# Kernel tuning notes

Hardware: AMD Instinct MI355X
Metric: run time of the kernel (lower is better)

Reference implementation:

```python
import jax, jax.numpy as jnp
import numpy as np

B, N, F = 2048, 65536, 128
NUM_K = 3
NUM_LABELS = 10
EXPONENT = 2.0


def setup_inputs() -> dict:
    key = jax.random.key(0)
    k1, k2, k3 = jax.random.split(key, 3)
    # positive inputs: tf.pow with a float exponent NaNs on negative bases
    x_input = jax.random.uniform(k1, (B, F), dtype=jnp.float32)
    train_inputs = jax.random.uniform(k2, (N, F), dtype=jnp.float32)
    train_labels = jax.random.randint(k3, (N,), 0, NUM_LABELS, dtype=jnp.int32)
    features = jnp.ones((F,), dtype=jnp.float32)  # abe_features, ones init
    return {
        "x_input": x_input,
        "train_inputs": train_inputs,
        "train_labels": train_labels,
        "features": features,
    }


def reference(x_input, train_inputs, train_labels, features):
    # weighted_inputs = features * train_inputs
    w = features[None, :] * train_inputs  # [N, F]

    # Minkowsky distance (faithful to the TF graph):
    # (sum(x^p) + sum(w^p))^(1/p) - 2 * x @ w^T
    left = jnp.sum(x_input ** EXPONENT, axis=1)[:, None]   # [B, 1]
    right = jnp.sum(w ** EXPONENT, axis=1)[None, :]        # [1, N]
    distance = (left + right) ** (1.0 / EXPONENT) - 2.0 * (x_input @ w.T)  # [B, N]

    # top-k nearest neighbors via top_k of negated distances
    values, indices = jax.lax.top_k(-distance, NUM_K)      # [B, K]

    # gather neighbor labels and average (tf.reduce_mean on int = floor div)
    labels = train_labels[indices]                          # [B, K] int32
    outputs = jnp.sum(labels, axis=1) // NUM_K              # [B] int32
    one_hot = jax.nn.one_hot(outputs, NUM_LABELS, dtype=jnp.float32)  # [B, NUM_LABELS]

    return (one_hot, values, indices, labels)
```

## Files before the change

### kernel.cpp

```cpp
#include <hip/hip_runtime.h>
#include <hip/hip_bf16.h>
#include <cstdint>
#include <cstddef>

typedef short bf16x8 __attribute__((ext_vector_type(8)));
typedef float f32x4 __attribute__((ext_vector_type(4)));

namespace {
constexpr int kB = 2048;
constexpr int kN = 65536;
constexpr int kF = 128;
constexpr int kLabels = 10;
constexpr int kIMax = 0x7fffffff;

constexpr int BM = 256;
constexpr int BN = 256;
constexpr int SLICE = 2048;
constexpr int NTILES = SLICE / BN;
constexpr int NCH = 12;
constexpr int NCHT = NTILES * NCH;
constexpr int NSUB = kN / 32;
constexpr float kMargin = 0.05f;
}

#define TOP3_INSERT(dd, ii, D0, I0, D1, I1, D2, I2)                              \
  do {                                                                           \
    float _d = (dd); int _i = (ii);                                              \
    if (_d < (D0) || (_d == (D0) && _i < (I0))) {                                \
      (D2) = (D1); (I2) = (I1); (D1) = (D0); (I1) = (I0); (D0) = _d; (I0) = _i;  \
    } else if (_d < (D1) || (_d == (D1) && _i < (I1))) {                         \
      (D2) = (D1); (I2) = (I1); (D1) = _d; (I1) = _i;                            \
    } else if (_d < (D2) || (_d == (D2) && _i < (I2))) {                         \
      (D2) = _d; (I2) = _i;                                                      \
    }                                                                            \
  } while (0)

__device__ inline unsigned short f2bf(float a) {
  __hip_bfloat16 h = __float2bfloat16(a);
  return __builtin_bit_cast(unsigned short, h);
}
__device__ inline float bf2f(unsigned short u) {
  return __bfloat162float(__builtin_bit_cast(__hip_bfloat16, u));
}

__device__ inline void gload_lds16(const void* g, void* l) {
  __builtin_amdgcn_global_load_lds(
      (const __attribute__((address_space(1))) void*)g,
      (__attribute__((address_space(3))) void*)l, 16, 0, 0);
}

__global__ __launch_bounds__(256) void pack_sumsq_kernel(
    const float* __restrict__ x, const float* __restrict__ train,
    const float* __restrict__ features, unsigned short* __restrict__ Ap,
    unsigned short* __restrict__ Bp, float* __restrict__ left,
    float* __restrict__ right) {
  const int wid = (int)((blockIdx.x * 256 + threadIdx.x) >> 6);
  const int lane = threadIdx.x & 63;
  if (wid >= kB + kN) return;
  const float2 fv = reinterpret_cast<const float2*>(features)[lane];
  const float* src;
  unsigned short* dst;
  float pm0, pm1, sm0, sm1;
  if (wid < kB) {
    src = x + (size_t)wid * kF;
    dst = Ap + (size_t)wid * 256;
    pm0 = fv.x; pm1 = fv.y;
    sm0 = 1.0f; sm1 = 1.0f;
  } else {
    src = train + (size_t)(wid - kB) * kF;
    dst = Bp + (size_t)(wid - kB) * 256;
    pm0 = 1.0f; pm1 = 1.0f;
    sm0 = fv.x; sm1 = fv.y;
  }
  const float2 v = reinterpret_cast<const float2*>(src)[lane];
  const float pa = v.x * pm0, pb = v.y * pm1;
  const float sa = v.x * sm0, sb = v.y * sm1;
  const unsigned short ha = f2bf(pa), hb = f2bf(pb);
  const unsigned short la = f2bf(pa - bf2f(ha)), lb = f2bf(pb - bf2f(hb));
  reinterpret_cast<unsigned int*>(dst)[lane] = (unsigned int)ha | ((unsigned int)hb << 16);
  reinterpret_cast<unsigned int*>(dst + 128)[lane] = (unsigned int)la | ((unsigned int)lb << 16);
  float s = sa * sa + sb * sb;
  #pragma unroll
  for (int m = 1; m <= 32; m <<= 1) s += __shfl_xor(s, m);
  if (lane == 0) {
    if (wid < kB) left[wid] = s;
    else right[wid - kB] = s;
  }
}

__global__ __launch_bounds__(512, 2) void knn_main_kernel(
    const unsigned short* __restrict__ Ap, const unsigned short* __restrict__ Bp,
    const float* __restrict__ left, const float* __restrict__ right,
    float* __restrict__ minbuf) {
  __shared__ alignas(16) unsigned short lsA[4][BM * 32];
  __shared__ alignas(16) unsigned short lsB[4][BN * 32];
  __shared__ alignas(16) float lsR[SLICE];

  const int slice = blockIdx.x;
  const int mb = blockIdx.y;
  const int row0 = mb * BM;
  const int col0 = slice * SLICE;
  const int t = threadIdx.x;
  const int lane = t & 63;
  const int wm = (t >> 6) >> 1;
  const int wn = (t >> 6) & 1;

  reinterpret_cast<float4*>(lsR)[t] =
      reinterpret_cast<const float4*>(right + col0)[t];

  float lrow[4][4];
  #pragma unroll
  for (int mf = 0; mf < 4; ++mf)
    #pragma unroll
    for (int rg = 0; rg < 4; ++rg)
      lrow[mf][rg] = left[row0 + wm * 64 + mf * 16 + (lane >> 4) * 4 + rg];

  const int rA = t >> 2;
  const int p = t & 3;
  size_t gbaseA[2], gbaseB[2];
  int ldsoff[2];
  #pragma unroll
  for (int i = 0; i < 2; ++i) {
    const int r = i * 128 + rA;
    const int ps = p ^ ((r >> 1) & 3);
    gbaseA[i] = (size_t)(row0 + r) * 512 + (size_t)ps * 16;
    gbaseB[i] = (size_t)(col0 + r) * 512 + (size_t)ps * 16;
    ldsoff[i] = i * 8192 + t * 16;
  }

  int offA[4], offB[8];
  #pragma unroll
  for (int mf = 0; mf < 4; ++mf) {
    const int rl = wm * 64 + mf * 16 + (lane & 15);
    offA[mf] = rl * 64 + (((lane >> 4) ^ ((rl >> 1) & 3)) * 16);
  }
  #pragma unroll
  for (int nf = 0; nf < 8; ++nf) {
    const int cl = wn * 128 + nf * 16 + (lane & 15);
    offB[nf] = cl * 64 + (((lane >> 4) ^ ((cl >> 1) & 3)) * 16);
  }

  const char* ApB = (const char*)Ap;
  const char* BpB = (const char*)Bp;

  auto stage = [&](int buf, int c, int nt) {
    const int skA = (c < 4) ? c * 32 : ((c < 8) ? 128 + (c - 4) * 32 : (c - 8) * 32);
    const int skB = (c < 4) ? c * 32 : ((c < 8) ? (c - 4) * 32 : 128 + (c - 8) * 32);
    char* lA = (char*)&lsA[buf][0];
    char* lB = (char*)&lsB[buf][0];
    #pragma unroll
    for (int i = 0; i < 2; ++i) {
      gload_lds16(ApB + gbaseA[i] + (size_t)skA * 2, lA + ldsoff[i]);
      gload_lds16(BpB + gbaseB[i] + (size_t)nt * 131072 + (size_t)skB * 2, lB + ldsoff[i]);
    }
  };

  asm volatile("s_waitcnt vmcnt(0) lgkmcnt(0)" ::: "memory");
  __syncthreads();

  int pn = 0, pc = 0;
  #pragma unroll
  for (int i = 0; i < 3; ++i) {
    stage(i, pc, pn);
    if (++pc == NCH) { pc = 0; ++pn; }
  }

  const bool bwriter = (lane & 3) == 0;

  int g = 0;
  for (int nt = 0; nt < NTILES; ++nt) {
    f32x4 acc[4][8];
    #pragma unroll
    for (int mf = 0; mf < 4; ++mf)
      #pragma unroll
      for (int nf = 0; nf < 8; ++nf)
        acc[mf][nf] = (f32x4){0.f, 0.f, 0.f, 0.f};

    for (int c = 0; c < NCH; ++c, ++g) {
      if (g + 3 < NCHT) {
        stage((g + 3) & 3, pc, pn);
        if (++pc == NCH) { pc = 0; ++pn; }
      }
      {
        const int rem = NCHT - 1 - g;
        if (rem >= 3)      asm volatile("s_waitcnt vmcnt(12)" ::: "memory");
        else if (rem == 2) asm volatile("s_waitcnt vmcnt(8)" ::: "memory");
        else if (rem == 1) asm volatile("s_waitcnt vmcnt(4)" ::: "memory");
        else               asm volatile("s_waitcnt vmcnt(0)" ::: "memory");
      }
      __builtin_amdgcn_s_barrier();
      asm volatile("" ::: "memory");

      const char* lA = (const char*)&lsA[g & 3][0];
      const char* lB = (const char*)&lsB[g & 3][0];
      bf16x8 a[4], b[8];
      #pragma unroll
      for (int mf = 0; mf < 4; ++mf)
        a[mf] = *reinterpret_cast<const bf16x8*>(lA + offA[mf]);
      #pragma unroll
      for (int nf = 0; nf < 8; ++nf)
        b[nf] = *reinterpret_cast<const bf16x8*>(lB + offB[nf]);
      __builtin_amdgcn_s_setprio(1);
      #pragma unroll
      for (int mf = 0; mf < 4; ++mf)
        #pragma unroll
        for (int nf = 0; nf < 8; ++nf)
          acc[mf][nf] = __builtin_amdgcn_mfma_f32_16x16x32_bf16(
              a[mf], b[nf], acc[mf][nf], 0, 0, 0);
      __builtin_amdgcn_s_setprio(0);
      asm volatile("" ::: "memory");
      __builtin_amdgcn_s_barrier();
      asm volatile("" ::: "memory");
    }

    float rj[8];
    #pragma unroll
    for (int nf = 0; nf < 8; ++nf)
      rj[nf] = lsR[nt * 256 + wn * 128 + nf * 16 + (lane & 15)];
    const int binbase = slice * 64 + nt * 8 + wn * 4 + ((lane >> 2) & 3);
    #pragma unroll
    for (int mf = 0; mf < 4; ++mf) {
      #pragma unroll
      for (int rg = 0; rg < 4; ++rg) {
        const float l = lrow[mf][rg];
        float d[8];
        #pragma unroll
        for (int nf = 0; nf < 8; ++nf)
          d[nf] = sqrtf(l + rj[nf]) - 2.0f * acc[mf][nf][rg];
        d[0] = fminf(d[0], d[4]); d[1] = fminf(d[1], d[5]);
        d[2] = fminf(d[2], d[6]); d[3] = fminf(d[3], d[7]);
        d[0] = fminf(d[0], d[2]); d[1] = fminf(d[1], d[3]);
        float v = fminf(d[0], d[1]);
        v = fminf(v, __shfl_xor(v, 1));
        v = fminf(v, __shfl_xor(v, 2));
        if (bwriter) {
          const int row = row0 + wm * 64 + mf * 16 + (lane >> 4) * 4 + rg;
          minbuf[(size_t)row * NSUB + binbase] = v;
        }
      }
    }
  }
}

__global__ __launch_bounds__(256) void select_rescore_kernel(
    const float* __restrict__ x, const float* __restrict__ train,
    const float* __restrict__ features, const float* __restrict__ left,
    const float* __restrict__ right, const int* __restrict__ labels,
    const float* __restrict__ minbuf, float* __restrict__ out) {
  __shared__ float Xs[4][kF];
  const int t = threadIdx.x;
  if (t < 128) {
    const int rr = t >> 5, q = t & 31;
    float4 xv = reinterpret_cast<const float4*>(
        x + (size_t)(blockIdx.x * 4 + rr) * kF)[q];
    const float4 f = reinterpret_cast<const float4*>(features)[q];
    xv.x *= f.x; xv.y *= f.y; xv.z *= f.z; xv.w *= f.w;
    reinterpret_cast<float4*>(&Xs[rr][0])[q] = xv;
  }
  __syncthreads();
  const int wave = t >> 6, lane = t & 63;
  const int row = blockIdx.x * 4 + wave;
  const float lr = left[row];
  const float* mrow = minbuf + (size_t)row * NSUB;

  float v0 = __builtin_inff(), v1 = v0, v2 = v0;
  #pragma unroll 4
  for (int i = 0; i < NSUB / 64; ++i) {
    const float m = mrow[i * 64 + lane];
    if (m < v0) { v2 = v1; v1 = v0; v0 = m; }
    else if (m < v1) { v2 = v1; v1 = m; }
    else if (m < v2) { v2 = m; }
  }
  #pragma unroll
  for (int msk = 1; msk <= 32; msk <<= 1) {
    const float e0 = __shfl_xor(v0, msk), e1 = __shfl_xor(v1, msk), e2 = __shfl_xor(v2, msk);
    if (e0 < v0) { v2 = v1; v1 = v0; v0 = e0; } else if (e0 < v1) { v2 = v1; v1 = e0; } else if (e0 < v2) v2 = e0;
    if (e1 < v0) { v2 = v1; v1 = v0; v0 = e1; } else if (e1 < v1) { v2 = v1; v1 = e1; } else if (e1 < v2) v2 = e1;
    if (e2 < v0) { v2 = v1; v1 = v0; v0 = e2; } else if (e2 < v1) { v2 = v1; v1 = e2; } else if (e2 < v2) v2 = e2;
  }
  const float tau = v2 + kMargin;

  float d0 = __builtin_inff(), d1 = d0, d2 = d0;
  int i0 = kIMax, i1 = kIMax, i2 = kIMax;
  for (int base = 0; base < NSUB; base += 64) {
    const float m = mrow[base + lane];
    unsigned long long msk = __ballot(m <= tau);
    while (msk) {
      const int bpos = __builtin_ctzll(msk);
      msk &= msk - 1;
      const int sub = base + bpos;
      if (lane < 32) {
        const int j = (sub >> 2) * 128 + (lane >> 2) * 16 + (sub & 3) * 4 + (lane & 3);
        const float4* wp = reinterpret_cast<const float4*>(train + (size_t)j * kF);
        float acc = 0.f;
        #pragma unroll 8
        for (int kq = 0; kq < 32; ++kq) {
          const float4 w4 = wp[kq];
          const float4 x4 = reinterpret_cast<const float4*>(&Xs[wave][0])[kq];
          acc = fmaf(x4.w, w4.w, fmaf(x4.z, w4.z, fmaf(x4.y, w4.y, fmaf(x4.x, w4.x, acc))));
        }
        const float d = sqrtf(lr + right[j]) - 2.0f * acc;
        TOP3_INSERT(d, j, d0, i0, d1, i1, d2, i2);
      }
    }
  }
  #pragma unroll
  for (int msk = 1; msk <= 32; msk <<= 1) {
    const float e0 = __shfl_xor(d0, msk), e1 = __shfl_xor(d1, msk), e2 = __shfl_xor(d2, msk);
    const int f0 = __shfl_xor(i0, msk), f1 = __shfl_xor(i1, msk), f2 = __shfl_xor(i2, msk);
    TOP3_INSERT(e0, f0, d0, i0, d1, i1, d2, i2);
    TOP3_INSERT(e1, f1, d0, i0, d1, i1, d2, i2);
    TOP3_INSERT(e2, f2, d0, i0, d1, i1, d2, i2);
  }
  if (lane == 0) {
    const int l0 = labels[i0], l1 = labels[i1], l2 = labels[i2];
    const int o = (l0 + l1 + l2) / 3;
    float* one_hot = out;
    float* values = out + (size_t)kB * kLabels;
    float* indices = values + (size_t)kB * 3;
    float* labs = indices + (size_t)kB * 3;
    #pragma unroll
    for (int c = 0; c < kLabels; ++c)
      one_hot[(size_t)row * kLabels + c] = (c == o) ? 1.0f : 0.0f;
    values[row * 3 + 0] = -d0; values[row * 3 + 1] = -d1; values[row * 3 + 2] = -d2;
    indices[row * 3 + 0] = (float)i0; indices[row * 3 + 1] = (float)i1; indices[row * 3 + 2] = (float)i2;
    labs[row * 3 + 0] = (float)l0; labs[row * 3 + 1] = (float)l1; labs[row * 3 + 2] = (float)l2;
  }
}

extern "C" void kernel_launch(void* const* d_in, const int* in_sizes, int n_in,
                              void* d_out, int out_size, void* d_ws, size_t ws_size,
                              hipStream_t stream) {
  const float* x = (const float*)d_in[0];
  const float* train = (const float*)d_in[1];
  const int* labels = (const int*)d_in[2];
  const float* features = (const float*)d_in[3];
  float* out = (float*)d_out;

  char* ws = (char*)d_ws;
  unsigned short* Bp = (unsigned short*)ws;
  unsigned short* Ap = (unsigned short*)(ws + 33554432);
  float* left = (float*)(ws + 34603008);
  float* right = (float*)(ws + 34611200);
  float* minbuf = (float*)(ws + 34873344);

  pack_sumsq_kernel<<<((kB + kN) * 64 + 255) / 256, 256, 0, stream>>>(
      x, train, features, Ap, Bp, left, right);
  knn_main_kernel<<<dim3(32, 8), 512, 0, stream>>>(Ap, Bp, left, right, minbuf);
  select_rescore_kernel<<<kB / 4, 256, 0, stream>>>(
      x, train, features, left, right, labels, minbuf, out);
}
```

Measured before the change: 299.2 us.

## Drop bf16 low part of train matrix, use two-term split-bf16 GEMM

The train matrix is now packed as a single bf16 high part, while the query matrix keeps its hi+lo split. This removes the third MFMA term (A_hi*B_lo), so the chunk count drops from 12 to 8 and the Bp workspace is halved. The LDS pipeline is restructured to triple-buffer pairs of A hi/lo chunks that share one B chunk, so each B load feeds two MFMA passes. Distances become less accurate because the train values carry bf16 rounding error, which relies on the rescore margin to keep top-k exact.

```diff
diff --git a/kernel.cpp b/kernel.cpp
--- a/kernel.cpp
+++ b/kernel.cpp
@@ -17,8 +17,8 @@
 constexpr int BN = 256;
 constexpr int SLICE = 2048;
 constexpr int NTILES = SLICE / BN;
-constexpr int NCH = 12;
-constexpr int NCHT = NTILES * NCH;
+constexpr int NKQ = 4;
+constexpr int NPAIRS = NTILES * NKQ;
 constexpr int NSUB = kN / 32;
 constexpr float kMargin = 0.05f;
 }
@@ -61,14 +61,17 @@
   const float* src;
   unsigned short* dst;
   float pm0, pm1, sm0, sm1;
+  bool isA;
   if (wid < kB) {
+    isA = true;
     src = x + (size_t)wid * kF;
     dst = Ap + (size_t)wid * 256;
     pm0 = fv.x; pm1 = fv.y;
     sm0 = 1.0f; sm1 = 1.0f;
   } else {
+    isA = false;
     src = train + (size_t)(wid - kB) * kF;
-    dst = Bp + (size_t)(wid - kB) * 256;
+    dst = Bp + (size_t)(wid - kB) * 128;
     pm0 = 1.0f; pm1 = 1.0f;
     sm0 = fv.x; sm1 = fv.y;
   }
@@ -76,9 +79,11 @@
   const float pa = v.x * pm0, pb = v.y * pm1;
   const float sa = v.x * sm0, sb = v.y * sm1;
   const unsigned short ha = f2bf(pa), hb = f2bf(pb);
-  const unsigned short la = f2bf(pa - bf2f(ha)), lb = f2bf(pb - bf2f(hb));
   reinterpret_cast<unsigned int*>(dst)[lane] = (unsigned int)ha | ((unsigned int)hb << 16);
-  reinterpret_cast<unsigned int*>(dst + 128)[lane] = (unsigned int)la | ((unsigned int)lb << 16);
+  if (isA) {
+    const unsigned short la = f2bf(pa - bf2f(ha)), lb = f2bf(pb - bf2f(hb));
+    reinterpret_cast<unsigned int*>(dst + 128)[lane] = (unsigned int)la | ((unsigned int)lb << 16);
+  }
   float s = sa * sa + sb * sb;
   #pragma unroll
   for (int m = 1; m <= 32; m <<= 1) s += __shfl_xor(s, m);
@@ -92,8 +97,8 @@
     const unsigned short* __restrict__ Ap, const unsigned short* __restrict__ Bp,
     const float* __restrict__ left, const float* __restrict__ right,
     float* __restrict__ minbuf) {
-  __shared__ alignas(16) unsigned short lsA[4][BM * 32];
-  __shared__ alignas(16) unsigned short lsB[4][BN * 32];
+  __shared__ alignas(16) unsigned short lsA[3][BM * 64];
+  __shared__ alignas(16) unsigned short lsB[3][BN * 32];
   __shared__ alignas(16) float lsR[SLICE];
 
   const int slice = blockIdx.x;
@@ -124,7 +129,7 @@
     const int r = i * 128 + rA;
     const int ps = p ^ ((r >> 1) & 3);
     gbaseA[i] = (size_t)(row0 + r) * 512 + (size_t)ps * 16;
-    gbaseB[i] = (size_t)(col0 + r) * 512 + (size_t)ps * 16;
+    gbaseB[i] = (size_t)(col0 + r) * 256 + (size_t)ps * 16;
     ldsoff[i] = i * 8192 + t * 16;
   }
 
@@ -143,27 +148,22 @@
   const char* ApB = (const char*)Ap;
   const char* BpB = (const char*)Bp;
 
-  auto stage = [&](int buf, int c, int nt) {
-    const int skA = (c < 4) ? c * 32 : ((c < 8) ? 128 + (c - 4) * 32 : (c - 8) * 32);
-    const int skB = (c < 4) ? c * 32 : ((c < 8) ? (c - 4) * 32 : 128 + (c - 8) * 32);
+  auto stage = [&](int buf, int kq, int nt) {
     char* lA = (char*)&lsA[buf][0];
     char* lB = (char*)&lsB[buf][0];
     #pragma unroll
     for (int i = 0; i < 2; ++i) {
-      gload_lds16(ApB + gbaseA[i] + (size_t)skA * 2, lA + ldsoff[i]);
-      gload_lds16(BpB + gbaseB[i] + (size_t)nt * 131072 + (size_t)skB * 2, lB + ldsoff[i]);
+      gload_lds16(ApB + gbaseA[i] + (size_t)kq * 64, lA + ldsoff[i]);
+      gload_lds16(ApB + gbaseA[i] + 256 + (size_t)kq * 64, lA + 16384 + ldsoff[i]);
+      gload_lds16(BpB + gbaseB[i] + (size_t)nt * 65536 + (size_t)kq * 64, lB + ldsoff[i]);
     }
   };
 
   asm volatile("s_waitcnt vmcnt(0) lgkmcnt(0)" ::: "memory");
   __syncthreads();
 
-  int pn = 0, pc = 0;
-  #pragma unroll
-  for (int i = 0; i < 3; ++i) {
-    stage(i, pc, pn);
-    if (++pc == NCH) { pc = 0; ++pn; }
-  }
+  stage(0, 0, 0);
+  stage(1, 1, 0);
 
   const bool bwriter = (lane & 3) == 0;
 
@@ -176,27 +176,23 @@
       for (int nf = 0; nf < 8; ++nf)
         acc[mf][nf] = (f32x4){0.f, 0.f, 0.f, 0.f};
 
-    for (int c = 0; c < NCH; ++c, ++g) {
-      if (g + 3 < NCHT) {
-        stage((g + 3) & 3, pc, pn);
-        if (++pc == NCH) { pc = 0; ++pn; }
-      }
-      {
-        const int rem = NCHT - 1 - g;
-        if (rem >= 3)      asm volatile("s_waitcnt vmcnt(12)" ::: "memory");
-        else if (rem == 2) asm volatile("s_waitcnt vmcnt(8)" ::: "memory");
-        else if (rem == 1) asm volatile("s_waitcnt vmcnt(4)" ::: "memory");
-        else               asm volatile("s_waitcnt vmcnt(0)" ::: "memory");
-      }
+    for (int kq = 0; kq < NKQ; ++kq, ++g) {
+      if (g + 2 < NPAIRS)
+        stage((g + 2) % 3, (g + 2) & 3, (g + 2) >> 2);
+      if (g < NPAIRS - 2)      asm volatile("s_waitcnt vmcnt(12)" ::: "memory");
+      else if (g == NPAIRS - 2) asm volatile("s_waitcnt vmcnt(6)" ::: "memory");
+      else                      asm volatile("s_waitcnt vmcnt(0)" ::: "memory");
       __builtin_amdgcn_s_barrier();
       asm volatile("" ::: "memory");
 
-      const char* lA = (const char*)&lsA[g & 3][0];
-      const char* lB = (const char*)&lsB[g & 3][0];
-      bf16x8 a[4], b[8];
-      #pragma unroll
-      for (int mf = 0; mf < 4; ++mf)
-        a[mf] = *reinterpret_cast<const bf16x8*>(lA + offA[mf]);
+      const char* lA = (const char*)&lsA[g % 3][0];
+      const char* lB = (const char*)&lsB[g % 3][0];
+      bf16x8 a0[4], a1[4], b[8];
+      #pragma unroll
+      for (int mf = 0; mf < 4; ++mf) {
+        a0[mf] = *reinterpret_cast<const bf16x8*>(lA + offA[mf]);
+        a1[mf] = *reinterpret_cast<const bf16x8*>(lA + 16384 + offA[mf]);
+      }
       #pragma unroll
       for (int nf = 0; nf < 8; ++nf)
         b[nf] = *reinterpret_cast<const bf16x8*>(lB + offB[nf]);
@@ -206,7 +202,13 @@
         #pragma unroll
         for (int nf = 0; nf < 8; ++nf)
           acc[mf][nf] = __builtin_amdgcn_mfma_f32_16x16x32_bf16(
-              a[mf], b[nf], acc[mf][nf], 0, 0, 0);
+              a0[mf], b[nf], acc[mf][nf], 0, 0, 0);
+      #pragma unroll
+      for (int mf = 0; mf < 4; ++mf)
+        #pragma unroll
+        for (int nf = 0; nf < 8; ++nf)
+          acc[mf][nf] = __builtin_amdgcn_mfma_f32_16x16x32_bf16(
+              a1[mf], b[nf], acc[mf][nf], 0, 0, 0);
       __builtin_amdgcn_s_setprio(0);
       asm volatile("" ::: "memory");
       __builtin_amdgcn_s_barrier();
@@ -339,10 +341,10 @@
 
   char* ws = (char*)d_ws;
   unsigned short* Bp = (unsigned short*)ws;
-  unsigned short* Ap = (unsigned short*)(ws + 33554432);
-  float* left = (float*)(ws + 34603008);
-  float* right = (float*)(ws + 34611200);
-  float* minbuf = (float*)(ws + 34873344);
+  unsigned short* Ap = (unsigned short*)(ws + 16777216);
+  float* left = (float*)(ws + 17825792);
+  float* right = (float*)(ws + 17833984);
+  float* minbuf = (float*)(ws + 18874368);
 
   pack_sumsq_kernel<<<((kB + kN) * 64 + 255) / 256, 256, 0, stream>>>(
       x, train, features, Ap, Bp, left, right);
```

After: 343.4 us. +14.8%, slower.

## Halve M tile to 128 rows with 256-thread blocks and triple-buffered LDS pipeline

Applied to the files above, without the earlier changes.

Shrinks the main GEMM/top-k block from 256x256 with 8 waves to 128x256 with 4 waves, doubling the grid to 32x16 blocks. The LDS ring drops from 4 to 3 stages with prefetch distance 2, and the staging loads and vmcnt waits are reworked to match. The goal is less LDS per block and more blocks per CU so latency is hidden better. The cost is half the reuse of each B tile per block, which doubles global/L2 traffic for the train matrix, and a shallower prefetch.

```diff
diff --git a/kernel.cpp b/kernel.cpp
--- a/kernel.cpp
+++ b/kernel.cpp
@@ -13,7 +13,7 @@
 constexpr int kLabels = 10;
 constexpr int kIMax = 0x7fffffff;
 
-constexpr int BM = 256;
+constexpr int BM = 128;
 constexpr int BN = 256;
 constexpr int SLICE = 2048;
 constexpr int NTILES = SLICE / BN;
@@ -88,12 +88,12 @@
   }
 }
 
-__global__ __launch_bounds__(512, 2) void knn_main_kernel(
+__global__ __launch_bounds__(256, 2) void knn_main_kernel(
     const unsigned short* __restrict__ Ap, const unsigned short* __restrict__ Bp,
     const float* __restrict__ left, const float* __restrict__ right,
     float* __restrict__ minbuf) {
-  __shared__ alignas(16) unsigned short lsA[4][BM * 32];
-  __shared__ alignas(16) unsigned short lsB[4][BN * 32];
+  __shared__ alignas(16) unsigned short lsA[3][BM * 32];
+  __shared__ alignas(16) unsigned short lsB[3][BN * 32];
   __shared__ alignas(16) float lsR[SLICE];
 
   const int slice = blockIdx.x;
@@ -105,8 +105,10 @@
   const int wm = (t >> 6) >> 1;
   const int wn = (t >> 6) & 1;
 
-  reinterpret_cast<float4*>(lsR)[t] =
-      reinterpret_cast<const float4*>(right + col0)[t];
+  #pragma unroll
+  for (int i = 0; i < 2; ++i)
+    reinterpret_cast<float4*>(lsR)[t + i * 256] =
+        reinterpret_cast<const float4*>(right + col0)[t + i * 256];
 
   float lrow[4][4];
   #pragma unroll
@@ -115,17 +117,23 @@
     for (int rg = 0; rg < 4; ++rg)
       lrow[mf][rg] = left[row0 + wm * 64 + mf * 16 + (lane >> 4) * 4 + rg];
 
-  const int rA = t >> 2;
+  const int rr = t >> 2;
   const int p = t & 3;
-  size_t gbaseA[2], gbaseB[2];
-  int ldsoff[2];
+  size_t gbaseA[2], gbaseB[4];
+  int ldsoffA[2], ldsoffB[4];
   #pragma unroll
   for (int i = 0; i < 2; ++i) {
-    const int r = i * 128 + rA;
+    const int r = i * 64 + rr;
     const int ps = p ^ ((r >> 1) & 3);
     gbaseA[i] = (size_t)(row0 + r) * 512 + (size_t)ps * 16;
+    ldsoffA[i] = i * 4096 + t * 16;
+  }
+  #pragma unroll
+  for (int i = 0; i < 4; ++i) {
+    const int r = i * 64 + rr;
+    const int ps = p ^ ((r >> 1) & 3);
     gbaseB[i] = (size_t)(col0 + r) * 512 + (size_t)ps * 16;
-    ldsoff[i] = i * 8192 + t * 16;
+    ldsoffB[i] = i * 4096 + t * 16;
   }
 
   int offA[4], offB[8];
@@ -149,21 +157,18 @@
     char* lA = (char*)&lsA[buf][0];
     char* lB = (char*)&lsB[buf][0];
     #pragma unroll
-    for (int i = 0; i < 2; ++i) {
-      gload_lds16(ApB + gbaseA[i] + (size_t)skA * 2, lA + ldsoff[i]);
-      gload_lds16(BpB + gbaseB[i] + (size_t)nt * 131072 + (size_t)skB * 2, lB + ldsoff[i]);
-    }
+    for (int i = 0; i < 2; ++i)
+      gload_lds16(ApB + gbaseA[i] + (size_t)skA * 2, lA + ldsoffA[i]);
+    #pragma unroll
+    for (int i = 0; i < 4; ++i)
+      gload_lds16(BpB + gbaseB[i] + (size_t)nt * 131072 + (size_t)skB * 2, lB + ldsoffB[i]);
   };
 
   asm volatile("s_waitcnt vmcnt(0) lgkmcnt(0)" ::: "memory");
   __syncthreads();
 
-  int pn = 0, pc = 0;
-  #pragma unroll
-  for (int i = 0; i < 3; ++i) {
-    stage(i, pc, pn);
-    if (++pc == NCH) { pc = 0; ++pn; }
-  }
+  stage(0, 0, 0);
+  stage(1, 1, 0);
 
   const bool bwriter = (lane & 3) == 0;
 
@@ -177,22 +182,16 @@
         acc[mf][nf] = (f32x4){0.f, 0.f, 0.f, 0.f};
 
     for (int c = 0; c < NCH; ++c, ++g) {
-      if (g + 3 < NCHT) {
-        stage((g + 3) & 3, pc, pn);
-        if (++pc == NCH) { pc = 0; ++pn; }
-      }
-      {
-        const int rem = NCHT - 1 - g;
-        if (rem >= 3)      asm volatile("s_waitcnt vmcnt(12)" ::: "memory");
-        else if (rem == 2) asm volatile("s_waitcnt vmcnt(8)" ::: "memory");
-        else if (rem == 1) asm volatile("s_waitcnt vmcnt(4)" ::: "memory");
-        else               asm volatile("s_waitcnt vmcnt(0)" ::: "memory");
-      }
+      if (g + 2 < NCHT)
+        stage((g + 2) % 3, (g + 2) % NCH, (g + 2) / NCH);
+      if (g <= NCHT - 3)       asm volatile("s_waitcnt vmcnt(12)" ::: "memory");
+      else if (g == NCHT - 2)  asm volatile("s_waitcnt vmcnt(6)" ::: "memory");
+      else                     asm volatile("s_waitcnt vmcnt(0)" ::: "memory");
       __builtin_amdgcn_s_barrier();
       asm volatile("" ::: "memory");
 
-      const char* lA = (const char*)&lsA[g & 3][0];
-      const char* lB = (const char*)&lsB[g & 3][0];
+      const char* lA = (const char*)&lsA[g % 3][0];
+      const char* lB = (const char*)&lsB[g % 3][0];
       bf16x8 a[4], b[8];
       #pragma unroll
       for (int mf = 0; mf < 4; ++mf)
@@ -346,7 +345,7 @@
 
   pack_sumsq_kernel<<<((kB + kN) * 64 + 255) / 256, 256, 0, stream>>>(
       x, train, features, Ap, Bp, left, right);
-  knn_main_kernel<<<dim3(32, 8), 512, 0, stream>>>(Ap, Bp, left, right, minbuf);
+  knn_main_kernel<<<dim3(32, 16), 256, 0, stream>>>(Ap, Bp, left, right, minbuf);
   select_rescore_kernel<<<kB / 4, 256, 0, stream>>>(
       x, train, features, left, right, labels, minbuf, out);
 }
```

Measured after the change: 288.9 us. -3.4%, faster.
